# Performance work log

Hardware: AMD Instinct MI355X
Metric: run time of the kernel (lower is better)

The kernel has to match this reference:

```python
import jax, jax.numpy as jnp
import numpy as np

B, DIM_IN, DIM_OUT, K, EMBED, N, S = 32, 32, 32, 2, 16, 2048, 12


def setup_inputs() -> dict:
    key = jax.random.key(0)
    ks = jax.random.split(key, 12)
    sc = 0.1
    return {
        "x": jax.random.normal(ks[0], (B, DIM_IN, N, S), dtype=jnp.float32),
        "node_embeddings": jax.random.normal(ks[1], (N, EMBED), dtype=jnp.float32),
        "node_embeddings2": jax.random.normal(ks[2], (N, EMBED), dtype=jnp.float32),
        "weights_pool": jax.random.normal(ks[3], (EMBED, K + 1, DIM_IN, DIM_OUT), dtype=jnp.float32) * sc,
        "weights_pool2": jax.random.normal(ks[4], (EMBED, K + 1, DIM_IN, DIM_OUT), dtype=jnp.float32) * sc,
        "bias_pool": jax.random.normal(ks[5], (EMBED, DIM_OUT), dtype=jnp.float32) * sc,
        "bias_pool2": jax.random.normal(ks[6], (EMBED, DIM_OUT), dtype=jnp.float32) * sc,
        "fc0_w": jax.random.normal(ks[7], (1, S), dtype=jnp.float32) * sc,
        "fc0_b": jnp.zeros((1,), dtype=jnp.float32),
        "fc1_w": jax.random.normal(ks[8], (EMBED, N), dtype=jnp.float32) * sc,
        "fc1_b": jnp.zeros((EMBED,), dtype=jnp.float32),
        "fc2_w": jax.random.normal(ks[9], (EMBED, DIM_IN), dtype=jnp.float32) * sc,
        "fc2_b": jnp.zeros((EMBED,), dtype=jnp.float32),
    }


def _mlp(x, fc0_w, fc0_b, fc1_w, fc1_b, fc2_w, fc2_b):
    # x: [B, i, n, s] -> use first batch element, as in the torch code
    h = x[0]                                        # [i, n, s]
    h = jnp.tanh((h @ fc0_w.T + fc0_b).squeeze(-1))  # [i, n]
    h = jnp.tanh(h @ fc1_w.T + fc1_b)                # [i, d]
    h = h.T                                          # [d, i]
    h = jnp.tanh(h @ fc2_w.T + fc2_b)                # [d, d]
    return h


def reference(x, node_embeddings, node_embeddings2, weights_pool, weights_pool2,
              bias_pool, bias_pool2, fc0_w, fc0_b, fc1_w, fc1_b, fc2_w, fc2_b):
    m = _mlp(x, fc0_w, fc0_b, fc1_w, fc1_b, fc2_w, fc2_b)          # [d, d]
    logits = jax.nn.relu((node_embeddings @ m) @ node_embeddings2.T)  # [n, n]
    support = jax.nn.softmax(logits, axis=1)                        # [n, n]

    # k-hop powers of the dynamic adjacency (k is a small static int)
    support_set = [jnp.eye(N, dtype=support.dtype)]
    for _ in range(K):
        support_set.append(support_set[-1] @ support)
    supports = jnp.stack(support_set, axis=0)                       # [K+1, n, n]

    # node-embedding-generated weights and bias
    weights = (jnp.einsum('nd,dkio->nkio', node_embeddings, weights_pool)
               + jnp.einsum('nd,dkio->nkio', node_embeddings2, weights_pool2))  # [n,K+1,i,o]
    bias = node_embeddings @ bias_pool + node_embeddings2 @ bias_pool2          # [n, o]

    x_g = jnp.einsum('knm,bims->bknis', supports, x)                # [b,K+1,n,i,s]
    x_gconv = jnp.einsum('bknis,nkio->bsno', x_g, weights) + bias   # [b,s,n,o]
    out = jnp.transpose(x_gconv, (0, 3, 2, 1))                      # [b,o,n,s]
    # dropout is identity in eval mode
    return out
```

## Files before the change

### kernel.cpp

```cpp
#include <hip/hip_runtime.h>


typedef float  f32x4  __attribute__((ext_vector_type(4)));
typedef __bf16 bf16x8 __attribute__((ext_vector_type(8)));
typedef unsigned short u16;

#define GLOAD16(gp, lp) __builtin_amdgcn_global_load_lds( \
    (const __attribute__((address_space(1))) void*)(gp),  \
    (__attribute__((address_space(3))) void*)(lp), 16, 0, 0)

__device__ __forceinline__ u16 f2bf(float f){
  union { float f; unsigned u; } v; v.f = f;
  unsigned u = v.u;
  u += 0x7fffu + ((u >> 16) & 1u);
  return (u16)(u >> 16);
}
__device__ __forceinline__ float bf2f(u16 h){
  union { unsigned u; float f; } v; v.u = ((unsigned)h) << 16;
  return v.f;
}
__device__ __forceinline__ float2 unp2(unsigned u){
  union { unsigned q; float f; } a, b;
  a.q = u << 16; b.q = u & 0xffff0000u;
  return make_float2(a.f, b.f);
}

__global__ void k_h1(const float* __restrict__ x, const float* __restrict__ fc0w,
                     const float* __restrict__ fc0b, float* __restrict__ h1){
  int g = blockIdx.x * 256 + threadIdx.x;
  const float* xp = x + (long)g * 12;
  float s = fc0b[0];
  #pragma unroll
  for (int j = 0; j < 12; j++) s += xp[j] * fc0w[j];
  h1[g] = tanhf(s);
}

__global__ __launch_bounds__(256) void k_h2a(const float* __restrict__ h1,
                                             const float* __restrict__ fc1w,
                                             float* __restrict__ h2raw){
  __shared__ float red[4];
  int id = blockIdx.x;
  int i = id >> 4, d = id & 15;
  int t = threadIdx.x;
  const float* hp = h1 + i * 2048;
  const float* wp = fc1w + d * 2048;
  float s = 0.f;
  for (int nn = t; nn < 2048; nn += 256) s += hp[nn] * wp[nn];
  for (int off = 32; off > 0; off >>= 1) s += __shfl_down(s, off, 64);
  if ((t & 63) == 0) red[t >> 6] = s;
  __syncthreads();
  if (t == 0) h2raw[id] = red[0] + red[1] + red[2] + red[3];
}

__global__ void k_h2b(const float* __restrict__ h2raw, const float* __restrict__ fc1b,
                      const float* __restrict__ fc2w, const float* __restrict__ fc2b,
                      float* __restrict__ mmat){
  __shared__ float h2[512];
  int t = threadIdx.x;
  {
    int d = t & 15;
    h2[t] = tanhf(h2raw[t] + fc1b[d]);
  }
  __syncthreads();
  if (t < 256){
    int dd = t >> 4, e = t & 15;
    float s2 = fc2b[e];
    #pragma unroll
    for (int ii = 0; ii < 32; ii++) s2 += h2[ii * 16 + dd] * fc2w[e * 32 + ii];
    mmat[dd * 16 + e] = tanhf(s2);
  }
}

__global__ __launch_bounds__(256) void k_support(const float* __restrict__ E1,
                                                 const float* __restrict__ E2,
                                                 const float* __restrict__ mmat,
                                                 u16* __restrict__ sup){
  __shared__ float ml[256];
  __shared__ float tv[16];
  __shared__ float red[8];
  int n = blockIdx.x, t = threadIdx.x;
  ml[t] = mmat[t];
  __syncthreads();
  if (t < 16){
    float s = 0.f;
    const float* er = E1 + n * 16;
    #pragma unroll
    for (int d = 0; d < 16; d++) s += er[d] * ml[d * 16 + t];
    tv[t] = s;
  }
  __syncthreads();
  float lmax = -1e30f;
  float lv[8];
  #pragma unroll
  for (int p = 0; p < 8; p++){
    int j = t + p * 256;
    const float* e2 = E2 + j * 16;
    float s = 0.f;
    #pragma unroll
    for (int d = 0; d < 16; d++) s += tv[d] * e2[d];
    s = fmaxf(s, 0.f);
    lv[p] = s;
    lmax = fmaxf(lmax, s);
  }
  for (int off = 32; off > 0; off >>= 1) lmax = fmaxf(lmax, __shfl_down(lmax, off, 64));
  if ((t & 63) == 0) red[t >> 6] = lmax;
  __syncthreads();
  if (t == 0) red[0] = fmaxf(fmaxf(red[0], red[1]), fmaxf(red[2], red[3]));
  __syncthreads();
  float mx = red[0];
  float lsum = 0.f;
  #pragma unroll
  for (int p = 0; p < 8; p++){ float e = __expf(lv[p] - mx); lv[p] = e; lsum += e; }
  for (int off = 32; off > 0; off >>= 1) lsum += __shfl_down(lsum, off, 64);
  if ((t & 63) == 0) red[4 + (t >> 6)] = lsum;
  __syncthreads();
  if (t == 0) red[4] = red[4] + red[5] + red[6] + red[7];
  __syncthreads();
  float inv = 1.f / red[4];
  #pragma unroll
  for (int p = 0; p < 8; p++) sup[(long)n * 2048 + t + p * 256] = f2bf(lv[p] * inv);
}

__global__ __launch_bounds__(256) void k_xbt2(const float* __restrict__ x,
                                              u16* __restrict__ Xb,
                                              u16* __restrict__ Xbt){
  __shared__ u16 tile[64][65];
  int cT = blockIdx.x * 64;
  int mT = blockIdx.y * 64;
  int t = threadIdx.x;
  int r = t >> 6, cc = t & 63;
  int cg = cT + cc;
  int bi = cg / 12, s = cg - bi * 12;
  long xoff = (long)bi * 24576 + s;
  #pragma unroll
  for (int p = 0; p < 16; p++){
    int rr = p * 4 + r;
    u16 v = f2bf(x[xoff + (long)(mT + rr) * 12]);
    tile[rr][cc] = v;
    Xb[(long)(mT + rr) * 12288 + cg] = v;
  }
  __syncthreads();
  #pragma unroll
  for (int p = 0; p < 16; p++){
    int rr = p * 4 + r;
    Xbt[(long)(cT + rr) * 2048 + mT + cc] = tile[cc][rr];
  }
}

__global__ __launch_bounds__(256) void k_wb2(const float* __restrict__ E1, const float* __restrict__ E2,
                                             const float* __restrict__ P1, const float* __restrict__ P2,
                                             const float* __restrict__ BP1, const float* __restrict__ BP2,
                                             float* __restrict__ W, float* __restrict__ biasN){
  int bid = blockIdx.x, t = threadIdx.x;
  if (bid < 6144){
    int nb = bid & 511, rb = bid >> 9;
    int n = nb * 4 + (t >> 6);
    int r4 = rb * 64 + (t & 63);
    const float* e1 = E1 + n * 16;
    const float* e2 = E2 + n * 16;
    f32x4 s = {0.f, 0.f, 0.f, 0.f};
    #pragma unroll
    for (int d = 0; d < 16; d++){
      f32x4 p1 = *(const f32x4*)(P1 + d * 3072 + r4 * 4);
      f32x4 p2 = *(const f32x4*)(P2 + d * 3072 + r4 * 4);
      s += p1 * e1[d] + p2 * e2[d];
    }
    *(f32x4*)(W + (long)n * 3072 + r4 * 4) = s;
  } else {
    int e = (bid - 6144) * 256 + t;
    int n = e >> 5, o = e & 31;
    const float* e1 = E1 + n * 16;
    const float* e2 = E2 + n * 16;
    float s = 0.f;
    #pragma unroll
    for (int d = 0; d < 16; d++) s += e1[d] * BP1[d * 32 + o] + e2[d] * BP2[d * 32 + o];
    biasN[e] = s;
  }
}

__global__ __launch_bounds__(512, 4) void k_gemm(const u16* __restrict__ A,
                                                 const u16* __restrict__ Bt,
                                                 u16* __restrict__ Cd,
                                                 u16* __restrict__ Ct,
                                                 int writeT){
  __shared__ u16 lds[40960];
  int tid  = threadIdx.x;
  int wave = tid >> 6, lane = tid & 63;
  int l15 = lane & 15, q = lane >> 4, l7 = l15 & 7;
  int wm = wave >> 2, wn = wave & 3;

  int lin  = blockIdx.y * 64 + blockIdx.x;
  int xcd  = lin & 7;
  int slot = lin >> 3;
  int yN   = slot >> 3;
  int xN   = (slot & 7) * 8 + xcd;
  long mBase = (long)yN * 128;
  long cBase = (long)xN * 192;

  f32x4 acc[4][3];
  #pragma unroll
  for (int t2 = 0; t2 < 4; t2++)
    #pragma unroll
    for (int u2 = 0; u2 < 3; u2++) acc[t2][u2] = (f32x4){0.f, 0.f, 0.f, 0.f};

  int Lrow = tid >> 3;
  int cel  = (tid & 7) ^ (Lrow & 7);
  const u16* gAp = A  + (mBase + Lrow) * 2048 + cel * 8;
  const u16* gBp = Bt + (cBase + Lrow) * 2048 + cel * 8;

#define GL_A(nx, ko, r) GLOAD16(gAp + (r) * (64 * 2048) + (ko), \
                                lds + (nx) + (r) * 4096 + wave * 512)
#define GL_B(nx, ko, r) GLOAD16(gBp + (r) * (64 * 2048) + (ko), \
                                lds + (nx) + 8192 + (r) * 4096 + wave * 512)

#define LDA(dst) do { \
    _Pragma("unroll") \
    for (int t2 = 0; t2 < 4; t2++){ \
      int row = wm * 64 + t2 * 16 + l15; \
      _Pragma("unroll") \
      for (int kk = 0; kk < 2; kk++) \
        dst[t2][kk] = *(const bf16x8*)&lds[bA + row * 64 + (((kk << 2) | q) ^ l7) * 8]; \
    } } while(0)

#define LDB(dst, j) do { \
    _Pragma("unroll") \
    for (int kk = 0; kk < 2; kk++) \
      dst[kk] = *(const bf16x8*)&lds[bB + ((j) * 64 + wn * 16 + l15) * 64 + (((kk << 2) | q) ^ l7) * 8]; \
  } while(0)

#define MFMA_Q(AF, BB, j) do { \
    __builtin_amdgcn_s_setprio(1); \
    _Pragma("unroll") \
    for (int t2 = 0; t2 < 4; t2++) \
      _Pragma("unroll") \
      for (int kk = 0; kk < 2; kk++) \
        acc[t2][(j)] = __builtin_amdgcn_mfma_f32_16x16x32_bf16( \
            AF[t2][kk], BB[kk], acc[t2][(j)], 0, 0, 0); \
    __builtin_amdgcn_s_setprio(0); \
  } while(0)

  GL_A(0, 0, 0); GL_A(0, 0, 1); GL_B(0, 0, 0);
  GL_B(0, 0, 1); GL_B(0, 0, 2);

  for (int t = 0; t < 32; t++){
    const int bufo = (t & 1) ? 20480 : 0;
    const int bA = bufo;
    const int bB = bufo + 8192;
    const int nx = 20480 - bufo;
    const long ko = (long)(t + 1) * 64;
    bf16x8 aA[4][2], bb0[2], bb1[2], bb2[2];
    asm volatile("s_waitcnt vmcnt(0)" ::: "memory");
    __builtin_amdgcn_s_barrier();
    LDA(aA);
    LDB(bb0, 0);
    LDB(bb1, 1);
    LDB(bb2, 2);
    if (t < 31){ GL_A(nx, ko, 0); GL_A(nx, ko, 1); GL_B(nx, ko, 0); }
    MFMA_Q(aA, bb0, 0);
    if (t < 31){ GL_B(nx, ko, 1); }
    MFMA_Q(aA, bb1, 1);
    if (t < 31){ GL_B(nx, ko, 2); }
    MFMA_Q(aA, bb2, 2);
  }
  asm volatile("s_waitcnt vmcnt(0)" ::: "memory");
  __builtin_amdgcn_sched_barrier(0);
  __syncthreads();

  #pragma unroll
  for (int t2 = 0; t2 < 4; t2++){
    int m0 = wm * 64 + t2 * 16 + q * 4;
    #pragma unroll
    for (int j = 0; j < 3; j++){
      int lc = j * 64 + wn * 16 + l15;
      ushort4 v = make_ushort4(f2bf(acc[t2][j][0]), f2bf(acc[t2][j][1]),
                               f2bf(acc[t2][j][2]), f2bf(acc[t2][j][3]));
      int sw = ((m0 >> 3) ^ (lc & 7) ^ ((lc >> 3) & 7));
      *(ushort4*)&lds[lc * 128 + (sw << 3) + (m0 & 7)] = v;
    }
  }
  __syncthreads();
  if (writeT){
    int rr0 = tid >> 4;
    int ch  = tid & 15;
    #pragma unroll
    for (int p = 0; p < 6; p++){
      int r = p * 32 + rr0;
      int sw = (ch ^ (r & 7) ^ ((r >> 3) & 7));
      uint4 v = *(const uint4*)&lds[r * 128 + (sw << 3)];
      *(uint4*)&Ct[(cBase + r) * 2048 + mBase + ch * 8] = v;
    }
  }
  {
    int rr = tid >> 5;
    int ch = tid & 31;
    if (ch < 24){
      #pragma unroll
      for (int p = 0; p < 8; p++){
        int m = p * 16 + rr;
        int msw = (m >> 3), ml = m & 7;
        unsigned w[4];
        #pragma unroll
        for (int jj = 0; jj < 4; jj++){
          int c0 = ch * 8 + jj * 2, c1 = c0 + 1;
          unsigned lo = lds[c0 * 128 + (((msw ^ (c0 & 7) ^ ((c0 >> 3) & 7)) << 3)) + ml];
          unsigned hi = lds[c1 * 128 + (((msw ^ (c1 & 7) ^ ((c1 >> 3) & 7)) << 3)) + ml];
          w[jj] = lo | (hi << 16);
        }
        uint4 v = make_uint4(w[0], w[1], w[2], w[3]);
        *(uint4*)&Cd[(mBase + m) * 12288 + cBase + ch * 8] = v;
      }
    }
  }
#undef GL_A
#undef GL_B
#undef LDA
#undef LDB
#undef MFMA_Q
}

__global__ __launch_bounds__(256, 4) void k_final(const u16* __restrict__ G0,
                                                  const u16* __restrict__ G1,
                                                  const u16* __restrict__ G2,
                                                  const float* __restrict__ W,
                                                  const float* __restrict__ biasN,
                                                  float* __restrict__ out){
  __shared__ __align__(16) u16 gs[32 * 400];
  __shared__ __align__(16) float ws4[1024];
  __shared__ float bbuf[32];
  int bid = blockIdx.x;
  int n = (bid & 7) * 256 + (bid >> 3);
  int t = threadIdx.x;
  int b = t >> 3, oc = t & 7;
  f32x4 acc[4][3];
  #pragma unroll
  for (int jo = 0; jo < 4; jo++)
    #pragma unroll
    for (int v = 0; v < 3; v++) acc[jo][v] = (f32x4){0.f, 0.f, 0.f, 0.f};

  const u16* srcs[3] = {G0, G1, G2};
  for (int k = 0; k < 3; k++){
    __syncthreads();
    const uint4* src = (const uint4*)(srcs[k] + (long)n * 12288);
    #pragma unroll
    for (int p = 0; p < 6; p++){
      int c = t + p * 256;
      int br = c / 48, wi = c - br * 48;
      *(uint4*)&gs[br * 400 + wi * 8] = src[c];
    }
    const float4* wsrc = (const float4*)(W + (long)n * 3072 + k * 1024);
    *(float4*)&ws4[t * 4] = wsrc[t];
    if (k == 0 && t < 8) *(float4*)&bbuf[t * 4] = ((const float4*)(biasN + (long)n * 32))[t];
    __syncthreads();

    const u16* gp = gs + b * 400;
    #pragma unroll 4
    for (int ii = 0; ii < 16; ii++){
      uint4 A  = *(const uint4*)&gp[ii * 24];
      uint4 Bc = *(const uint4*)&gp[ii * 24 + 8];
      uint4 Cc = *(const uint4*)&gp[ii * 24 + 16];
      float2 p0 = unp2(A.x),  p1 = unp2(A.y),  p2 = unp2(A.z),  p3 = unp2(A.w);
      float2 p4 = unp2(Bc.x), p5 = unp2(Bc.y), p6 = unp2(Bc.z), p7 = unp2(Bc.w);
      float2 p8 = unp2(Cc.x), p9 = unp2(Cc.y), pa = unp2(Cc.z), pb = unp2(Cc.w);
      f32x4 G0v0 = (f32x4){p0.x, p0.y, p1.x, p1.y};
      f32x4 G0v1 = (f32x4){p2.x, p2.y, p3.x, p3.y};
      f32x4 G0v2 = (f32x4){p4.x, p4.y, p5.x, p5.y};
      f32x4 G1v0 = (f32x4){p6.x, p6.y, p7.x, p7.y};
      f32x4 G1v1 = (f32x4){p8.x, p8.y, p9.x, p9.y};
      f32x4 G1v2 = (f32x4){pa.x, pa.y, pb.x, pb.y};
      #pragma unroll
      for (int jo = 0; jo < 4; jo++){
        float w0 = ws4[(ii * 2)     * 32 + oc + jo * 8];
        float w1 = ws4[(ii * 2 + 1) * 32 + oc + jo * 8];
        acc[jo][0] += G0v0 * w0;
        acc[jo][1] += G0v1 * w0;
        acc[jo][2] += G0v2 * w0;
        acc[jo][0] += G1v0 * w1;
        acc[jo][1] += G1v1 * w1;
        acc[jo][2] += G1v2 * w1;
      }
    }
  }
  #pragma unroll
  for (int jo = 0; jo < 4; jo++){
    int o = oc + jo * 8;
    float bv = bbuf[o];
    f32x4 bs = {bv, bv, bv, bv};
    long base = ((long)(b * 32 + o) * 2048 + n) * 12;
    *(f32x4*)(out + base)     = acc[jo][0] + bs;
    *(f32x4*)(out + base + 4) = acc[jo][1] + bs;
    *(f32x4*)(out + base + 8) = acc[jo][2] + bs;
  }
}

extern "C" void kernel_launch(void* const* d_in, const int* in_sizes, int n_in,
                              void* d_out, int out_size, void* d_ws, size_t ws_size,
                              hipStream_t stream){
  const float* x    = (const float*)d_in[0];
  const float* E1   = (const float*)d_in[1];
  const float* E2   = (const float*)d_in[2];
  const float* P1   = (const float*)d_in[3];
  const float* P2   = (const float*)d_in[4];
  const float* BP1  = (const float*)d_in[5];
  const float* BP2  = (const float*)d_in[6];
  const float* fc0w = (const float*)d_in[7];
  const float* fc0b = (const float*)d_in[8];
  const float* fc1w = (const float*)d_in[9];
  const float* fc1b = (const float*)d_in[10];
  const float* fc2w = (const float*)d_in[11];
  const float* fc2b = (const float*)d_in[12];
  float* out = (float*)d_out;

  char* ws = (char*)d_ws;
  size_t off = 0;
  auto carve = [&](size_t bytes) -> char* {
    char* p = ws + off;
    off += (bytes + 255) & ~(size_t)255;
    return p;
  };
  float* h1            = (float*)carve((size_t)65536 * 4);
  float* h2raw         = (float*)carve((size_t)512 * 4);
  float* mmat          = (float*)carve((size_t)256 * 4);
  u16* sup             = (u16*)carve((size_t)2048 * 2048 * 2);
  u16* Xbt             = (u16*)carve((size_t)12288 * 2048 * 2);
  u16* Xb              = (u16*)carve((size_t)2048 * 12288 * 2);
  u16* G1t             = (u16*)carve((size_t)12288 * 2048 * 2);
  u16* G1              = (u16*)carve((size_t)2048 * 12288 * 2);
  float* W             = (float*)carve((size_t)2048 * 3072 * 4);
  float* biasN         = (float*)carve((size_t)2048 * 32 * 4);
  u16* G2              = Xbt;
  (void)ws_size; (void)in_sizes; (void)n_in; (void)out_size;

  k_h1     <<<256, 256, 0, stream>>>(x, fc0w, fc0b, h1);
  k_h2a    <<<512, 256, 0, stream>>>(h1, fc1w, h2raw);
  k_h2b    <<<1, 512, 0, stream>>>(h2raw, fc1b, fc2w, fc2b, mmat);
  k_support<<<2048, 256, 0, stream>>>(E1, E2, mmat, sup);
  k_xbt2   <<<dim3(192, 32), 256, 0, stream>>>(x, Xb, Xbt);
  k_wb2    <<<6400, 256, 0, stream>>>(E1, E2, P1, P2, BP1, BP2, W, biasN);
  k_gemm   <<<dim3(64, 16), 512, 0, stream>>>(sup, Xbt, G1, G1t, 1);
  k_gemm   <<<dim3(64, 16), 512, 0, stream>>>(sup, G1t, G2, G1t, 0);
  k_final  <<<2048, 256, 0, stream>>>(Xb, G1, G2, W, biasN, out);
}
```

Baseline: 557.4 us.

## Vectorize x transpose kernel and read G operands directly from global in final

The transpose/convert kernel now reads x with contiguous float4 loads across a whole batch-element slab, stages the bf16 values in a large shared tile, and writes both Xb and Xbt with 16-byte stores instead of strided scalar accesses. The final kernel drops its shared-memory staging of the G rows and loads them directly from global memory, with occupancy raised to 6 blocks per CU. This targets uncoalesced memory traffic in the transpose and shared-memory/sync overhead in the final kernel. The risk is a larger LDS footprint per transpose block and less-coalesced per-thread global reads in the final kernel.

```diff
diff --git a/kernel.cpp b/kernel.cpp
--- a/kernel.cpp
+++ b/kernel.cpp
@@ -121,29 +121,46 @@
   for (int p = 0; p < 8; p++) sup[(long)n * 2048 + t + p * 256] = f2bf(lv[p] * inv);
 }
 
-__global__ __launch_bounds__(256) void k_xbt2(const float* __restrict__ x,
+__global__ __launch_bounds__(256) void k_xbt3(const float* __restrict__ x,
                                               u16* __restrict__ Xb,
                                               u16* __restrict__ Xbt){
-  __shared__ u16 tile[64][65];
-  int cT = blockIdx.x * 64;
-  int mT = blockIdx.y * 64;
+  __shared__ u16 tile[64 * 392];
+  int biG = blockIdx.x * 32;
+  int cB  = blockIdx.x * 384;
+  int mT  = blockIdx.y * 64;
   int t = threadIdx.x;
-  int r = t >> 6, cc = t & 63;
-  int cg = cT + cc;
-  int bi = cg / 12, s = cg - bi * 12;
-  long xoff = (long)bi * 24576 + s;
-  #pragma unroll
-  for (int p = 0; p < 16; p++){
-    int rr = p * 4 + r;
-    u16 v = f2bf(x[xoff + (long)(mT + rr) * 12]);
-    tile[rr][cc] = v;
-    Xb[(long)(mT + rr) * 12288 + cg] = v;
-  }
-  __syncthreads();
-  #pragma unroll
-  for (int p = 0; p < 16; p++){
-    int rr = p * 4 + r;
-    Xbt[(long)(cT + rr) * 2048 + mT + cc] = tile[cc][rr];
+  #pragma unroll
+  for (int p = 0; p < 24; p++){
+    int idx = t + p * 256;
+    int bl = idx / 192;
+    int f4 = idx - bl * 192;
+    float4 v = *(const float4*)(x + ((long)(biG + bl) * 2048 + mT) * 12 + f4 * 4);
+    int ml = f4 / 3;
+    int s0 = (f4 - ml * 3) * 4;
+    ushort4 h = make_ushort4(f2bf(v.x), f2bf(v.y), f2bf(v.z), f2bf(v.w));
+    *(ushort4*)&tile[ml * 392 + bl * 12 + s0] = h;
+  }
+  __syncthreads();
+  #pragma unroll
+  for (int p = 0; p < 12; p++){
+    int idx = t + p * 256;
+    int m = idx / 48, u4 = idx - m * 48;
+    uint4 v = *(const uint4*)&tile[m * 392 + u4 * 8];
+    *(uint4*)&Xb[(long)(mT + m) * 12288 + cB + u4 * 8] = v;
+  }
+  #pragma unroll
+  for (int p = 0; p < 12; p++){
+    int idx = t + p * 256;
+    int cl = idx >> 3, oct = idx & 7;
+    int m0 = oct * 8;
+    unsigned w[4];
+    #pragma unroll
+    for (int jj = 0; jj < 4; jj++){
+      unsigned lo = tile[(m0 + jj * 2    ) * 392 + cl];
+      unsigned hi = tile[(m0 + jj * 2 + 1) * 392 + cl];
+      w[jj] = lo | (hi << 16);
+    }
+    *(uint4*)&Xbt[(long)(cB + cl) * 2048 + mT + m0] = make_uint4(w[0], w[1], w[2], w[3]);
   }
 }
 
@@ -318,13 +335,12 @@
 #undef MFMA_Q
 }
 
-__global__ __launch_bounds__(256, 4) void k_final(const u16* __restrict__ G0,
+__global__ __launch_bounds__(256, 6) void k_final(const u16* __restrict__ G0,
                                                   const u16* __restrict__ G1,
                                                   const u16* __restrict__ G2,
                                                   const float* __restrict__ W,
                                                   const float* __restrict__ biasN,
                                                   float* __restrict__ out){
-  __shared__ __align__(16) u16 gs[32 * 400];
   __shared__ __align__(16) float ws4[1024];
   __shared__ float bbuf[32];
   int bid = blockIdx.x;
@@ -340,19 +356,12 @@
   const u16* srcs[3] = {G0, G1, G2};
   for (int k = 0; k < 3; k++){
     __syncthreads();
-    const uint4* src = (const uint4*)(srcs[k] + (long)n * 12288);
-    #pragma unroll
-    for (int p = 0; p < 6; p++){
-      int c = t + p * 256;
-      int br = c / 48, wi = c - br * 48;
-      *(uint4*)&gs[br * 400 + wi * 8] = src[c];
-    }
     const float4* wsrc = (const float4*)(W + (long)n * 3072 + k * 1024);
     *(float4*)&ws4[t * 4] = wsrc[t];
     if (k == 0 && t < 8) *(float4*)&bbuf[t * 4] = ((const float4*)(biasN + (long)n * 32))[t];
     __syncthreads();
 
-    const u16* gp = gs + b * 400;
+    const u16* gp = srcs[k] + (long)n * 12288 + b * 384;
     #pragma unroll 4
     for (int ii = 0; ii < 16; ii++){
       uint4 A  = *(const uint4*)&gp[ii * 24];
@@ -434,7 +443,7 @@
   k_h2a    <<<512, 256, 0, stream>>>(h1, fc1w, h2raw);
   k_h2b    <<<1, 512, 0, stream>>>(h2raw, fc1b, fc2w, fc2b, mmat);
   k_support<<<2048, 256, 0, stream>>>(E1, E2, mmat, sup);
-  k_xbt2   <<<dim3(192, 32), 256, 0, stream>>>(x, Xb, Xbt);
+  k_xbt3   <<<dim3(32, 32), 256, 0, stream>>>(x, Xb, Xbt);
   k_wb2    <<<6400, 256, 0, stream>>>(E1, E2, P1, P2, BP1, BP2, W, biasN);
   k_gemm   <<<dim3(64, 16), 512, 0, stream>>>(sup, Xbt, G1, G1t, 1);
   k_gemm   <<<dim3(64, 16), 512, 0, stream>>>(sup, G1t, G2, G1t, 0);
```

Measured after the change: 1.233 ms. 2.21x slower.
